# Performance work log

Hardware: AMD Instinct MI355X
Metric: run time of the kernel (lower is better)

## Reference

```python
import jax, jax.numpy as jnp
import numpy as np

PS = 32

def _masks(ps):
    yy, xx = np.meshgrid(np.arange(ps), np.arange(ps), indexing='ij')
    c = (ps - 1) / 2.0
    r = np.sqrt((yy - c) ** 2 + (xx - c) ** 2)
    rm = max(r.max(), 1.0)
    ml = (r <= rm / 3.0).astype(np.float32)
    mm = ((r > rm / 3.0) & (r <= 2.0 * rm / 3.0)).astype(np.float32)
    mh = (r > 2.0 * rm / 3.0).astype(np.float32)
    return jnp.asarray(ml), jnp.asarray(mm), jnp.asarray(mh)

MASK_L, MASK_M, MASK_H = _masks(PS)

def setup_inputs() -> dict:
    key = jax.random.key(0)
    ks = jax.random.split(key, 4)
    B, C, H, W = 16, 3, 256, 256
    d = PS * PS            # 1024
    hidden = int(d * 1.5)  # 1536
    c_f = 64
    return {
        'x': jax.random.normal(ks[0], (B, C, H, W), dtype=jnp.float32),
        'W1': jax.random.normal(ks[1], (d, hidden), dtype=jnp.float32) * 0.02,
        'b1': jnp.zeros((hidden,), jnp.float32),
        'W2': jax.random.normal(ks[2], (hidden, d), dtype=jnp.float32) * 0.02,
        'b2': jnp.zeros((d,), jnp.float32),
        'w_proj': jax.random.normal(ks[3], (c_f,), dtype=jnp.float32) * 0.5,
        'gamma': jnp.ones((c_f,), jnp.float32),
        'beta': jnp.zeros((c_f,), jnp.float32),
        'lf_gate': jnp.float32(0.33),
        'mf_gate': jnp.float32(0.34),
        'hf_gate': jnp.float32(0.33),
    }

def _forward(x, W1, b1, W2, b2, w_proj, gamma, beta, lf_gate, mf_gate, hf_gate):
    B, C, H, W = x.shape
    ps = PS
    gh, gw = H // ps, W // ps
    L = gh * gw
    # grayscale
    xg = 0.299 * x[:, 0] + 0.587 * x[:, 1] + 0.114 * x[:, 2]  # [B,H,W]
    # non-overlapping patchify (H,W multiples of ps -> no padding)
    pr = xg.reshape(B, gh, ps, gw, ps).transpose(0, 1, 3, 2, 4).reshape(B, L, ps, ps)
    # per-patch orthonormal FFT2 and magnitude
    mag = jnp.abs(jnp.fft.fft2(pr, norm='ortho'))  # [B,L,ps,ps]
    gate = (jax.nn.sigmoid(lf_gate) * MASK_L
            + jax.nn.sigmoid(mf_gate) * MASK_M
            + jax.nn.sigmoid(hf_gate) * MASK_H)
    mag = mag * gate
    mag_vec = mag.reshape(B * L, ps * ps)
    attn = jax.nn.sigmoid(jax.nn.relu(mag_vec @ W1 + b1) @ W2 + b2)
    mod = mag_vec * attn
    w = mod.mean(axis=-1).reshape(B, L, 1, 1)  # per-patch scalar weight
    recon = pr * (1.0 + w)
    # fold back (exact inverse of the reshape patchify)
    x_rec = recon.reshape(B, gh, gw, ps, ps).transpose(0, 1, 3, 2, 4).reshape(B, H, W)
    # 1x1 conv (1 -> c_f channels, no bias)
    out = x_rec[:, None, :, :] * w_proj[None, :, None, None]  # [B,c_f,H,W]
    # BatchNorm2d (training mode: batch stats, biased variance)
    mean = out.mean(axis=(0, 2, 3), keepdims=True)
    var = out.var(axis=(0, 2, 3), keepdims=True)
    out = (out - mean) * jax.lax.rsqrt(var + 1e-5)
    out = out * gamma[None, :, None, None] + beta[None, :, None, None]
    return jax.nn.relu(out)

def reference(x, W1, b1, W2, b2, w_proj, gamma, beta, lf_gate, mf_gate, hf_gate):
    return _forward(x, W1, b1, W2, b2, w_proj, gamma, beta, lf_gate, mf_gate, hf_gate)
```

## Files before the change

### kernel.cpp

```cpp
#include <hip/hip_runtime.h>
#include <hip/hip_bf16.h>
#include <math.h>

typedef __attribute__((ext_vector_type(8))) short bf16x8;
typedef __attribute__((ext_vector_type(4))) float f32x4;
typedef __attribute__((ext_vector_type(4))) unsigned short u16x4;

static __device__ __forceinline__ float bf2f(unsigned short u) {
    union { unsigned int i; float f; } v; v.i = ((unsigned int)u) << 16; return v.f;
}
static __device__ __forceinline__ unsigned short f2bf(float f) {
    union { float f; unsigned int i; } v; v.f = f;
    unsigned int x = v.i;
    return (unsigned short)((x + 0x7fffu + ((x >> 16) & 1u)) >> 16);
}
static __device__ __forceinline__ float sigmoidf(float v) {
    return 1.0f / (1.0f + expf(-v));
}
static __device__ __forceinline__ void gload16(const unsigned short* g, unsigned short* l) {
    __builtin_amdgcn_global_load_lds(
        (const __attribute__((address_space(1))) unsigned int*)g,
        (__attribute__((address_space(3))) unsigned int*)l, 16, 0, 0);
}

__global__ __launch_bounds__(256) void kpatch(
    const float* __restrict__ x, const float* __restrict__ lf,
    const float* __restrict__ mf, const float* __restrict__ hf,
    float* __restrict__ pr_out, unsigned short* __restrict__ mag_bf,
    float* __restrict__ ppsum, float* __restrict__ ppsq)
{
    __shared__ float sX[32][36];
    __shared__ float sYr[32][36];
    __shared__ float sYi[32][36];
    __shared__ float tc[32], ts[32];
    __shared__ float red_s[4], red_q[4];

    const int t = threadIdx.x;
    const int p = blockIdx.x;
    const int b = p >> 6, l = p & 63;
    const int gy = l >> 3, gx = l & 7;
    const int lane = t & 63, wave = t >> 6;

    if (t < 32) {
        float ang = (float)t * 0.19634954084936207f;
        tc[t] = cosf(ang);
        ts[t] = sinf(ang);
    }

    const int y  = t >> 3;
    const int xc = (t & 7) * 4;
    const int h  = gy * 32 + y;
    const int wbase = gx * 32 + xc;
    const long long idx0 = ((long long)(b * 3 + 0) * 256 + h) * 256 + wbase;
    const long long idx1 = ((long long)(b * 3 + 1) * 256 + h) * 256 + wbase;
    const long long idx2 = ((long long)(b * 3 + 2) * 256 + h) * 256 + wbase;
    float4 r4 = *(const float4*)(x + idx0);
    float4 g4 = *(const float4*)(x + idx1);
    float4 b4 = *(const float4*)(x + idx2);
    float4 gray;
    gray.x = 0.299f * r4.x + 0.587f * g4.x + 0.114f * b4.x;
    gray.y = 0.299f * r4.y + 0.587f * g4.y + 0.114f * b4.y;
    gray.z = 0.299f * r4.z + 0.587f * g4.z + 0.114f * b4.z;
    gray.w = 0.299f * r4.w + 0.587f * g4.w + 0.114f * b4.w;
    *(float4*)&sX[y][xc] = gray;
    *(float4*)(pr_out + p * 1024 + t * 4) = gray;

    float ls = gray.x + gray.y + gray.z + gray.w;
    float lq = gray.x * gray.x + gray.y * gray.y + gray.z * gray.z + gray.w * gray.w;
    #pragma unroll
    for (int off = 32; off > 0; off >>= 1) {
        ls += __shfl_down(ls, off, 64);
        lq += __shfl_down(lq, off, 64);
    }
    if (lane == 0) { red_s[wave] = ls; red_q[wave] = lq; }
    __syncthreads();
    if (t == 0) {
        ppsum[p] = red_s[0] + red_s[1] + red_s[2] + red_s[3];
        ppsq[p]  = red_q[0] + red_q[1] + red_q[2] + red_q[3];
    }

    {
        const int k  = t >> 3;
        const int c0 = (t & 7) * 4;
        float yr[4] = {0,0,0,0}, yi[4] = {0,0,0,0};
        for (int n = 0; n < 32; n++) {
            int wi = (k * n) & 31;
            float cw = tc[wi], sw = ts[wi];
            float4 xv = *(const float4*)&sX[n][c0];
            yr[0] += cw * xv.x; yi[0] -= sw * xv.x;
            yr[1] += cw * xv.y; yi[1] -= sw * xv.y;
            yr[2] += cw * xv.z; yi[2] -= sw * xv.z;
            yr[3] += cw * xv.w; yi[3] -= sw * xv.w;
        }
        *(float4*)&sYr[k][c0] = *(float4*)yr;
        *(float4*)&sYi[k][c0] = *(float4*)yi;
    }
    __syncthreads();

    {
        const int k  = t >> 3;
        const int m0 = (t & 7) * 4;
        float zr[4] = {0,0,0,0}, zi[4] = {0,0,0,0};
        for (int c = 0; c < 32; c++) {
            float yr = sYr[k][c];
            float yi = sYi[k][c];
            #pragma unroll
            for (int j = 0; j < 4; j++) {
                int wi = ((m0 + j) * c) & 31;
                float cw = tc[wi], sw = ts[wi];
                zr[j] += yr * cw + yi * sw;
                zi[j] += yi * cw - yr * sw;
            }
        }
        const float sl = sigmoidf(lf[0]);
        const float sm = sigmoidf(mf[0]);
        const float sh = sigmoidf(hf[0]);
        const float T1 = 480.5f / 9.0f;
        const float T2 = 4.0f * 480.5f / 9.0f;
        const float fk = (float)k - 15.5f;
        u16x4 outv;
        #pragma unroll
        for (int j = 0; j < 4; j++) {
            float fm = (float)(m0 + j) - 15.5f;
            float r2 = fk * fk + fm * fm;
            float g = (r2 <= T1) ? sl : ((r2 <= T2) ? sm : sh);
            float magv = sqrtf(zr[j] * zr[j] + zi[j] * zi[j]) * 0.03125f * g;
            outv[j] = f2bf(magv);
        }
        *(u16x4*)(mag_bf + p * 1024 + k * 32 + m0) = outv;
    }
}

__global__ __launch_bounds__(256) void kconvall(
    const float* __restrict__ W1, const float* __restrict__ W2,
    unsigned short* __restrict__ w1t, unsigned short* __restrict__ w2t)
{
    __shared__ float tile[32][33];
    int id = blockIdx.x;
    const float* W; unsigned short* WT; int K, N, k0, n0;
    if (id < 1536) {
        W = W1; WT = w1t; K = 1024; N = 1536;
        k0 = (id & 31) * 32; n0 = (id >> 5) * 32;
    } else {
        id -= 1536;
        W = W2; WT = w2t; K = 1536; N = 1024;
        k0 = (id % 48) * 32; n0 = (id / 48) * 32;
    }
    const int tx = threadIdx.x & 31, ty = threadIdx.x >> 5;
    #pragma unroll
    for (int i = 0; i < 4; i++) {
        int r = ty + i * 8;
        tile[r][tx] = W[(long long)(k0 + r) * N + n0 + tx];
    }
    __syncthreads();
    #pragma unroll
    for (int i = 0; i < 4; i++) {
        int r = ty + i * 8;
        WT[(long long)(n0 + r) * K + k0 + tx] = f2bf(tile[tx][r]);
    }
}

__global__ __launch_bounds__(256) void kgemm1(
    const unsigned short* __restrict__ A, const unsigned short* __restrict__ BT,
    const float* __restrict__ bias, unsigned short* __restrict__ C)
{
    const int K = 1024, N = 1536;
    __shared__ unsigned short sA[64 * 64];
    __shared__ unsigned short sB[64 * 64];

    const int t = threadIdx.x;
    const int lane = t & 63, wave = t >> 6;
    const int wm = wave & 1, wn = wave >> 1;
    const int m0 = blockIdx.x * 64, n0 = blockIdx.y * 64;

    const int u0 = t, u1 = t + 256;
    const int r0 = u0 >> 3, c0 = (u0 & 7) ^ (r0 & 7);
    const int r1 = u1 >> 3, c1 = (u1 & 7) ^ (r1 & 7);
    const unsigned short* agp0 = A  + (long long)(m0 + r0) * K + c0 * 8;
    const unsigned short* agp1 = A  + (long long)(m0 + r1) * K + c1 * 8;
    const unsigned short* bgp0 = BT + (long long)(n0 + r0) * K + c0 * 8;
    const unsigned short* bgp1 = BT + (long long)(n0 + r1) * K + c1 * 8;
    unsigned short* al0 = sA + u0 * 8;
    unsigned short* al1 = sA + u1 * 8;
    unsigned short* bl0 = sB + u0 * 8;
    unsigned short* bl1 = sB + u1 * 8;

    const int lr = lane & 15, quad = lane >> 4;
    const int ra0 = wm * 32 + lr, ra1 = ra0 + 16;
    const int rb0 = wn * 32 + lr, rb1 = rb0 + 16;
    const int ea = ra0 & 7, eb = rb0 & 7;

    f32x4 acc00 = {0,0,0,0}, acc01 = {0,0,0,0}, acc10 = {0,0,0,0}, acc11 = {0,0,0,0};

    for (int kk = 0; kk < K; kk += 64) {
        __syncthreads();
        gload16(agp0 + kk, al0);
        gload16(agp1 + kk, al1);
        gload16(bgp0 + kk, bl0);
        gload16(bgp1 + kk, bl1);
        __syncthreads();
        #pragma unroll
        for (int st = 0; st < 2; st++) {
            const int cq = st * 4 + quad;
            bf16x8 a0 = *(const bf16x8*)(sA + ra0 * 64 + ((cq ^ ea) << 3));
            bf16x8 a1 = *(const bf16x8*)(sA + ra1 * 64 + ((cq ^ ea) << 3));
            bf16x8 b0 = *(const bf16x8*)(sB + rb0 * 64 + ((cq ^ eb) << 3));
            bf16x8 b1 = *(const bf16x8*)(sB + rb1 * 64 + ((cq ^ eb) << 3));
            acc00 = __builtin_amdgcn_mfma_f32_16x16x32_bf16(a0, b0, acc00, 0, 0, 0);
            acc01 = __builtin_amdgcn_mfma_f32_16x16x32_bf16(a0, b1, acc01, 0, 0, 0);
            acc10 = __builtin_amdgcn_mfma_f32_16x16x32_bf16(a1, b0, acc10, 0, 0, 0);
            acc11 = __builtin_amdgcn_mfma_f32_16x16x32_bf16(a1, b1, acc11, 0, 0, 0);
        }
    }

    const int col0 = n0 + wn * 32 + lr, col1 = col0 + 16;
    const float bias0 = bias[col0], bias1 = bias[col1];
    const int row0b = m0 + wm * 32 + quad * 4;
    #pragma unroll
    for (int r = 0; r < 4; r++) {
        int row0 = row0b + r, row1 = row0 + 16;
        C[(long long)row0 * N + col0] = f2bf(fmaxf(acc00[r] + bias0, 0.0f));
        C[(long long)row0 * N + col1] = f2bf(fmaxf(acc01[r] + bias1, 0.0f));
        C[(long long)row1 * N + col0] = f2bf(fmaxf(acc10[r] + bias0, 0.0f));
        C[(long long)row1 * N + col1] = f2bf(fmaxf(acc11[r] + bias1, 0.0f));
    }
}

__global__ __launch_bounds__(256) void kgemm2d(
    const unsigned short* __restrict__ A, const unsigned short* __restrict__ BT,
    const float* __restrict__ bias, const unsigned short* __restrict__ mag,
    float* __restrict__ wpart)
{
    const int K = 1536;
    __shared__ unsigned short sA[64 * 64];
    __shared__ unsigned short sB[64 * 64];

    const int t = threadIdx.x;
    const int lane = t & 63, wave = t >> 6;
    const int wm = wave & 1, wn = wave >> 1;
    const int m0 = blockIdx.x * 64, n0 = blockIdx.y * 64;

    const int u0 = t, u1 = t + 256;
    const int r0 = u0 >> 3, c0 = (u0 & 7) ^ (r0 & 7);
    const int r1 = u1 >> 3, c1 = (u1 & 7) ^ (r1 & 7);
    const unsigned short* agp0 = A  + (long long)(m0 + r0) * K + c0 * 8;
    const unsigned short* agp1 = A  + (long long)(m0 + r1) * K + c1 * 8;
    const unsigned short* bgp0 = BT + (long long)(n0 + r0) * K + c0 * 8;
    const unsigned short* bgp1 = BT + (long long)(n0 + r1) * K + c1 * 8;
    unsigned short* al0 = sA + u0 * 8;
    unsigned short* al1 = sA + u1 * 8;
    unsigned short* bl0 = sB + u0 * 8;
    unsigned short* bl1 = sB + u1 * 8;

    const int lr = lane & 15, quad = lane >> 4;
    const int ra0 = wm * 32 + lr, ra1 = ra0 + 16;
    const int rb0 = wn * 32 + lr, rb1 = rb0 + 16;
    const int ea = ra0 & 7, eb = rb0 & 7;

    f32x4 acc00 = {0,0,0,0}, acc01 = {0,0,0,0}, acc10 = {0,0,0,0}, acc11 = {0,0,0,0};

    for (int kk = 0; kk < K; kk += 64) {
        __syncthreads();
        gload16(agp0 + kk, al0);
        gload16(agp1 + kk, al1);
        gload16(bgp0 + kk, bl0);
        gload16(bgp1 + kk, bl1);
        __syncthreads();
        #pragma unroll
        for (int st = 0; st < 2; st++) {
            const int cq = st * 4 + quad;
            bf16x8 a0 = *(const bf16x8*)(sA + ra0 * 64 + ((cq ^ ea) << 3));
            bf16x8 a1 = *(const bf16x8*)(sA + ra1 * 64 + ((cq ^ ea) << 3));
            bf16x8 b0 = *(const bf16x8*)(sB + rb0 * 64 + ((cq ^ eb) << 3));
            bf16x8 b1 = *(const bf16x8*)(sB + rb1 * 64 + ((cq ^ eb) << 3));
            acc00 = __builtin_amdgcn_mfma_f32_16x16x32_bf16(a0, b0, acc00, 0, 0, 0);
            acc01 = __builtin_amdgcn_mfma_f32_16x16x32_bf16(a0, b1, acc01, 0, 0, 0);
            acc10 = __builtin_amdgcn_mfma_f32_16x16x32_bf16(a1, b0, acc10, 0, 0, 0);
            acc11 = __builtin_amdgcn_mfma_f32_16x16x32_bf16(a1, b1, acc11, 0, 0, 0);
        }
    }

    const int col0 = n0 + wn * 32 + lr, col1 = col0 + 16;
    const float bias0 = bias[col0], bias1 = bias[col1];
    const int row0b = m0 + wm * 32 + quad * 4;

    float dsum0[4], dsum1[4];
    #pragma unroll
    for (int r = 0; r < 4; r++) {
        int row0 = row0b + r, row1 = row0 + 16;
        float v00 = sigmoidf(acc00[r] + bias0);
        float v01 = sigmoidf(acc01[r] + bias1);
        float v10 = sigmoidf(acc10[r] + bias0);
        float v11 = sigmoidf(acc11[r] + bias1);
        float m00 = bf2f(mag[(long long)row0 * 1024 + col0]);
        float m01 = bf2f(mag[(long long)row0 * 1024 + col1]);
        float m10 = bf2f(mag[(long long)row1 * 1024 + col0]);
        float m11 = bf2f(mag[(long long)row1 * 1024 + col1]);
        dsum0[r] = m00 * v00 + m01 * v01;
        dsum1[r] = m10 * v10 + m11 * v11;
    }
    #pragma unroll
    for (int r = 0; r < 4; r++) {
        #pragma unroll
        for (int mask = 8; mask > 0; mask >>= 1) {
            dsum0[r] += __shfl_xor(dsum0[r], mask, 64);
            dsum1[r] += __shfl_xor(dsum1[r], mask, 64);
        }
    }
    if (lr == 0) {
        const int cp = blockIdx.y * 2 + wn;
        #pragma unroll
        for (int r = 0; r < 4; r++) {
            wpart[(row0b + r) * 32 + cp]      = dsum0[r];
            wpart[(row0b + 16 + r) * 32 + cp] = dsum1[r];
        }
    }
}

__global__ __launch_bounds__(1024) void kfin(
    const float* __restrict__ wpart, const float* __restrict__ ppsum,
    const float* __restrict__ ppsq, const float* __restrict__ w_proj,
    const float* __restrict__ gamma, const float* __restrict__ beta,
    float* __restrict__ scales, float* __restrict__ der)
{
    __shared__ float rs[16], rq[16];
    const int p = threadIdx.x;
    const int lane = p & 63, wave = p >> 6;

    const float4* wp4 = (const float4*)(wpart + p * 32);
    float w = 0.0f;
    #pragma unroll
    for (int j = 0; j < 8; j++) {
        float4 v = wp4[j];
        w += v.x + v.y + v.z + v.w;
    }
    float scale = 1.0f + w * (1.0f / 1024.0f);
    scales[p] = scale;

    float s = scale * ppsum[p];
    float q = scale * scale * ppsq[p];
    #pragma unroll
    for (int off = 32; off > 0; off >>= 1) {
        s += __shfl_down(s, off, 64);
        q += __shfl_down(q, off, 64);
    }
    if (lane == 0) { rs[wave] = s; rq[wave] = q; }
    __syncthreads();
    if (p < 64) {
        float S = (p < 16) ? rs[p] : 0.0f;
        float Q = (p < 16) ? rq[p] : 0.0f;
        #pragma unroll
        for (int off = 8; off > 0; off >>= 1) {
            S += __shfl_down(S, off, 64);
            Q += __shfl_down(Q, off, 64);
        }
        S = __shfl(S, 0, 64);
        Q = __shfl(Q, 0, 64);
        const float invN = 1.0f / 1048576.0f;
        float mu  = S * invN;
        float var = Q * invN - mu * mu;
        float wp = w_proj[p];
        float A = wp * gamma[p] / sqrtf(wp * wp * var + 1e-5f);
        der[p]      = A;
        der[64 + p] = beta[p] - A * mu;
    }
}

__global__ __launch_bounds__(256) void kout(
    const float* __restrict__ pr, const float* __restrict__ scales,
    const float* __restrict__ der, float* __restrict__ out)
{
    const int total4 = 16777216;
    for (int i4 = blockIdx.x * 256 + threadIdx.x; i4 < total4; i4 += gridDim.x * 256) {
        const int w4 = i4 & 63;
        const int h = (i4 >> 6) & 255;
        const int plane = i4 >> 14;
        const int c = plane & 63;
        const int b = plane >> 6;
        const int p = (b << 6) + ((h >> 5) << 3) + (w4 >> 3);
        const int off4 = ((h & 31) << 3) + (w4 & 7);
        const float As = der[c] * scales[p];
        const float D2 = der[64 + c];
        float4 v = ((const float4*)pr)[p * 256 + off4];
        f32x4 o;
        o[0] = fmaxf(fmaf(As, v.x, D2), 0.0f);
        o[1] = fmaxf(fmaf(As, v.y, D2), 0.0f);
        o[2] = fmaxf(fmaf(As, v.z, D2), 0.0f);
        o[3] = fmaxf(fmaf(As, v.w, D2), 0.0f);
        __builtin_nontemporal_store(o, (f32x4*)out + i4);
    }
}

extern "C" void kernel_launch(void* const* d_in, const int* in_sizes, int n_in,
                              void* d_out, int out_size, void* d_ws, size_t ws_size,
                              hipStream_t stream)
{
    const float* x      = (const float*)d_in[0];
    const float* W1     = (const float*)d_in[1];
    const float* b1     = (const float*)d_in[2];
    const float* W2     = (const float*)d_in[3];
    const float* b2     = (const float*)d_in[4];
    const float* w_proj = (const float*)d_in[5];
    const float* gamma  = (const float*)d_in[6];
    const float* beta   = (const float*)d_in[7];
    const float* lf     = (const float*)d_in[8];
    const float* mf     = (const float*)d_in[9];
    const float* hf     = (const float*)d_in[10];

    char* ws = (char*)d_ws;
    float* pr                 = (float*)(ws);
    unsigned short* mag_bf    = (unsigned short*)(ws + (4u<<20));
    unsigned short* hidden_bf = (unsigned short*)(ws + (6u<<20));
    unsigned short* w1t       = (unsigned short*)(ws + (10u<<20));
    unsigned short* w2t       = (unsigned short*)(ws + (13u<<20));
    float* wpart              = (float*)(ws + (16u<<20));
    float* ppsum              = (float*)(ws + (17u<<20));
    float* ppsq               = (float*)(ws + (17u<<20) + 4096);
    float* scales             = (float*)(ws + (17u<<20) + 8192);
    float* der                = (float*)(ws + (17u<<20) + 12288);

    kconvall<<<3072, 256, 0, stream>>>(W1, W2, w1t, w2t);
    kpatch<<<1024, 256, 0, stream>>>(x, lf, mf, hf, pr, mag_bf, ppsum, ppsq);
    kgemm1<<<dim3(16, 24), 256, 0, stream>>>(mag_bf, w1t, b1, hidden_bf);
    kgemm2d<<<dim3(16, 16), 256, 0, stream>>>(hidden_bf, w2t, b2, mag_bf, wpart);
    kfin<<<1, 1024, 0, stream>>>(wpart, ppsum, ppsq, w_proj, gamma, beta, scales, der);
    kout<<<2048, 256, 0, stream>>>(pr, scales, der, (float*)d_out);
}
```

Baseline: 349.4 us.

## Merge weight conversion into patch kernel and double-buffer GEMM LDS tiles

Folds the W1/W2 transpose-to-bf16 conversion into the patch/FFT kernel as extra blocks, which removes one kernel launch and lets the two independent jobs run concurrently. Both GEMMs now double-buffer their shared-memory A/B tiles, issuing the next K-tile's global-to-LDS loads before computing on the current tile, so each iteration needs one barrier instead of two. This doubles LDS use per block, which may reduce occupancy. The merged kernel reuses the patch kernel's shared buffer as the transpose tile.

```diff
diff --git a/kernel.cpp b/kernel.cpp
--- a/kernel.cpp
+++ b/kernel.cpp
@@ -23,11 +23,13 @@
         (__attribute__((address_space(3))) unsigned int*)l, 16, 0, 0);
 }
 
-__global__ __launch_bounds__(256) void kpatch(
+__global__ __launch_bounds__(256) void kprep(
     const float* __restrict__ x, const float* __restrict__ lf,
     const float* __restrict__ mf, const float* __restrict__ hf,
+    const float* __restrict__ W1, const float* __restrict__ W2,
     float* __restrict__ pr_out, unsigned short* __restrict__ mag_bf,
-    float* __restrict__ ppsum, float* __restrict__ ppsq)
+    float* __restrict__ ppsum, float* __restrict__ ppsq,
+    unsigned short* __restrict__ w1t, unsigned short* __restrict__ w2t)
 {
     __shared__ float sX[32][36];
     __shared__ float sYr[32][36];
@@ -36,7 +38,36 @@
     __shared__ float red_s[4], red_q[4];
 
     const int t = threadIdx.x;
-    const int p = blockIdx.x;
+    const int bid = blockIdx.x;
+
+    if (bid >= 1024) {
+        int id = bid - 1024;
+        float (*tile)[33] = (float (*)[33])(&sX[0][0]);
+        const float* W; unsigned short* WT; int K, N, k0, n0;
+        if (id < 1536) {
+            W = W1; WT = w1t; K = 1024; N = 1536;
+            k0 = (id & 31) * 32; n0 = (id >> 5) * 32;
+        } else {
+            id -= 1536;
+            W = W2; WT = w2t; K = 1536; N = 1024;
+            k0 = (id % 48) * 32; n0 = (id / 48) * 32;
+        }
+        const int tx = t & 31, ty = t >> 5;
+        #pragma unroll
+        for (int i = 0; i < 4; i++) {
+            int r = ty + i * 8;
+            tile[r][tx] = W[(long long)(k0 + r) * N + n0 + tx];
+        }
+        __syncthreads();
+        #pragma unroll
+        for (int i = 0; i < 4; i++) {
+            int r = ty + i * 8;
+            WT[(long long)(n0 + r) * K + k0 + tx] = f2bf(tile[tx][r]);
+        }
+        return;
+    }
+
+    const int p = bid;
     const int b = p >> 6, l = p & 63;
     const int gy = l >> 3, gx = l & 7;
     const int lane = t & 63, wave = t >> 6;
@@ -131,42 +162,13 @@
     }
 }
 
-__global__ __launch_bounds__(256) void kconvall(
-    const float* __restrict__ W1, const float* __restrict__ W2,
-    unsigned short* __restrict__ w1t, unsigned short* __restrict__ w2t)
-{
-    __shared__ float tile[32][33];
-    int id = blockIdx.x;
-    const float* W; unsigned short* WT; int K, N, k0, n0;
-    if (id < 1536) {
-        W = W1; WT = w1t; K = 1024; N = 1536;
-        k0 = (id & 31) * 32; n0 = (id >> 5) * 32;
-    } else {
-        id -= 1536;
-        W = W2; WT = w2t; K = 1536; N = 1024;
-        k0 = (id % 48) * 32; n0 = (id / 48) * 32;
-    }
-    const int tx = threadIdx.x & 31, ty = threadIdx.x >> 5;
-    #pragma unroll
-    for (int i = 0; i < 4; i++) {
-        int r = ty + i * 8;
-        tile[r][tx] = W[(long long)(k0 + r) * N + n0 + tx];
-    }
-    __syncthreads();
-    #pragma unroll
-    for (int i = 0; i < 4; i++) {
-        int r = ty + i * 8;
-        WT[(long long)(n0 + r) * K + k0 + tx] = f2bf(tile[tx][r]);
-    }
-}
-
 __global__ __launch_bounds__(256) void kgemm1(
     const unsigned short* __restrict__ A, const unsigned short* __restrict__ BT,
     const float* __restrict__ bias, unsigned short* __restrict__ C)
 {
     const int K = 1024, N = 1536;
-    __shared__ unsigned short sA[64 * 64];
-    __shared__ unsigned short sB[64 * 64];
+    __shared__ unsigned short sA[2][64 * 64];
+    __shared__ unsigned short sB[2][64 * 64];
 
     const int t = threadIdx.x;
     const int lane = t & 63, wave = t >> 6;
@@ -180,10 +182,6 @@
     const unsigned short* agp1 = A  + (long long)(m0 + r1) * K + c1 * 8;
     const unsigned short* bgp0 = BT + (long long)(n0 + r0) * K + c0 * 8;
     const unsigned short* bgp1 = BT + (long long)(n0 + r1) * K + c1 * 8;
-    unsigned short* al0 = sA + u0 * 8;
-    unsigned short* al1 = sA + u1 * 8;
-    unsigned short* bl0 = sB + u0 * 8;
-    unsigned short* bl1 = sB + u1 * 8;
 
     const int lr = lane & 15, quad = lane >> 4;
     const int ra0 = wm * 32 + lr, ra1 = ra0 + 16;
@@ -192,25 +190,37 @@
 
     f32x4 acc00 = {0,0,0,0}, acc01 = {0,0,0,0}, acc10 = {0,0,0,0}, acc11 = {0,0,0,0};
 
+    gload16(agp0, sA[0] + u0 * 8);
+    gload16(agp1, sA[0] + u1 * 8);
+    gload16(bgp0, sB[0] + u0 * 8);
+    gload16(bgp1, sB[0] + u1 * 8);
+    __syncthreads();
+
+    int buf = 0;
     for (int kk = 0; kk < K; kk += 64) {
-        __syncthreads();
-        gload16(agp0 + kk, al0);
-        gload16(agp1 + kk, al1);
-        gload16(bgp0 + kk, bl0);
-        gload16(bgp1 + kk, bl1);
-        __syncthreads();
+        const int nx = kk + 64;
+        if (nx < K) {
+            gload16(agp0 + nx, sA[buf ^ 1] + u0 * 8);
+            gload16(agp1 + nx, sA[buf ^ 1] + u1 * 8);
+            gload16(bgp0 + nx, sB[buf ^ 1] + u0 * 8);
+            gload16(bgp1 + nx, sB[buf ^ 1] + u1 * 8);
+        }
+        const unsigned short* cA = sA[buf];
+        const unsigned short* cB = sB[buf];
         #pragma unroll
         for (int st = 0; st < 2; st++) {
             const int cq = st * 4 + quad;
-            bf16x8 a0 = *(const bf16x8*)(sA + ra0 * 64 + ((cq ^ ea) << 3));
-            bf16x8 a1 = *(const bf16x8*)(sA + ra1 * 64 + ((cq ^ ea) << 3));
-            bf16x8 b0 = *(const bf16x8*)(sB + rb0 * 64 + ((cq ^ eb) << 3));
-            bf16x8 b1 = *(const bf16x8*)(sB + rb1 * 64 + ((cq ^ eb) << 3));
+            bf16x8 a0 = *(const bf16x8*)(cA + ra0 * 64 + ((cq ^ ea) << 3));
+            bf16x8 a1 = *(const bf16x8*)(cA + ra1 * 64 + ((cq ^ ea) << 3));
+            bf16x8 b0 = *(const bf16x8*)(cB + rb0 * 64 + ((cq ^ eb) << 3));
+            bf16x8 b1 = *(const bf16x8*)(cB + rb1 * 64 + ((cq ^ eb) << 3));
             acc00 = __builtin_amdgcn_mfma_f32_16x16x32_bf16(a0, b0, acc00, 0, 0, 0);
             acc01 = __builtin_amdgcn_mfma_f32_16x16x32_bf16(a0, b1, acc01, 0, 0, 0);
             acc10 = __builtin_amdgcn_mfma_f32_16x16x32_bf16(a1, b0, acc10, 0, 0, 0);
             acc11 = __builtin_amdgcn_mfma_f32_16x16x32_bf16(a1, b1, acc11, 0, 0, 0);
         }
+        __syncthreads();
+        buf ^= 1;
     }
 
     const int col0 = n0 + wn * 32 + lr, col1 = col0 + 16;
@@ -232,8 +242,8 @@
     float* __restrict__ wpart)
 {
     const int K = 1536;
-    __shared__ unsigned short sA[64 * 64];
-    __shared__ unsigned short sB[64 * 64];
+    __shared__ unsigned short sA[2][64 * 64];
+    __shared__ unsigned short sB[2][64 * 64];
 
     const int t = threadIdx.x;
     const int lane = t & 63, wave = t >> 6;
@@ -247,10 +257,6 @@
     const unsigned short* agp1 = A  + (long long)(m0 + r1) * K + c1 * 8;
     const unsigned short* bgp0 = BT + (long long)(n0 + r0) * K + c0 * 8;
     const unsigned short* bgp1 = BT + (long long)(n0 + r1) * K + c1 * 8;
-    unsigned short* al0 = sA + u0 * 8;
-    unsigned short* al1 = sA + u1 * 8;
-    unsigned short* bl0 = sB + u0 * 8;
-    unsigned short* bl1 = sB + u1 * 8;
 
     const int lr = lane & 15, quad = lane >> 4;
     const int ra0 = wm * 32 + lr, ra1 = ra0 + 16;
@@ -259,25 +265,37 @@
 
     f32x4 acc00 = {0,0,0,0}, acc01 = {0,0,0,0}, acc10 = {0,0,0,0}, acc11 = {0,0,0,0};
 
+    gload16(agp0, sA[0] + u0 * 8);
+    gload16(agp1, sA[0] + u1 * 8);
+    gload16(bgp0, sB[0] + u0 * 8);
+    gload16(bgp1, sB[0] + u1 * 8);
+    __syncthreads();
+
+    int buf = 0;
     for (int kk = 0; kk < K; kk += 64) {
-        __syncthreads();
-        gload16(agp0 + kk, al0);
-        gload16(agp1 + kk, al1);
-        gload16(bgp0 + kk, bl0);
-        gload16(bgp1 + kk, bl1);
-        __syncthreads();
+        const int nx = kk + 64;
+        if (nx < K) {
+            gload16(agp0 + nx, sA[buf ^ 1] + u0 * 8);
+            gload16(agp1 + nx, sA[buf ^ 1] + u1 * 8);
+            gload16(bgp0 + nx, sB[buf ^ 1] + u0 * 8);
+            gload16(bgp1 + nx, sB[buf ^ 1] + u1 * 8);
+        }
+        const unsigned short* cA = sA[buf];
+        const unsigned short* cB = sB[buf];
         #pragma unroll
         for (int st = 0; st < 2; st++) {
             const int cq = st * 4 + quad;
-            bf16x8 a0 = *(const bf16x8*)(sA + ra0 * 64 + ((cq ^ ea) << 3));
-            bf16x8 a1 = *(const bf16x8*)(sA + ra1 * 64 + ((cq ^ ea) << 3));
-            bf16x8 b0 = *(const bf16x8*)(sB + rb0 * 64 + ((cq ^ eb) << 3));
-            bf16x8 b1 = *(const bf16x8*)(sB + rb1 * 64 + ((cq ^ eb) << 3));
+            bf16x8 a0 = *(const bf16x8*)(cA + ra0 * 64 + ((cq ^ ea) << 3));
+            bf16x8 a1 = *(const bf16x8*)(cA + ra1 * 64 + ((cq ^ ea) << 3));
+            bf16x8 b0 = *(const bf16x8*)(cB + rb0 * 64 + ((cq ^ eb) << 3));
+            bf16x8 b1 = *(const bf16x8*)(cB + rb1 * 64 + ((cq ^ eb) << 3));
             acc00 = __builtin_amdgcn_mfma_f32_16x16x32_bf16(a0, b0, acc00, 0, 0, 0);
             acc01 = __builtin_amdgcn_mfma_f32_16x16x32_bf16(a0, b1, acc01, 0, 0, 0);
             acc10 = __builtin_amdgcn_mfma_f32_16x16x32_bf16(a1, b0, acc10, 0, 0, 0);
             acc11 = __builtin_amdgcn_mfma_f32_16x16x32_bf16(a1, b1, acc11, 0, 0, 0);
         }
+        __syncthreads();
+        buf ^= 1;
     }
 
     const int col0 = n0 + wn * 32 + lr, col1 = col0 + 16;
@@ -419,8 +437,7 @@
     float* scales             = (float*)(ws + (17u<<20) + 8192);
     float* der                = (float*)(ws + (17u<<20) + 12288);
 
-    kconvall<<<3072, 256, 0, stream>>>(W1, W2, w1t, w2t);
-    kpatch<<<1024, 256, 0, stream>>>(x, lf, mf, hf, pr, mag_bf, ppsum, ppsq);
+    kprep<<<4096, 256, 0, stream>>>(x, lf, mf, hf, W1, W2, pr, mag_bf, ppsum, ppsq, w1t, w2t);
     kgemm1<<<dim3(16, 24), 256, 0, stream>>>(mag_bf, w1t, b1, hidden_bf);
     kgemm2d<<<dim3(16, 16), 256, 0, stream>>>(hidden_bf, w2t, b2, mag_bf, wpart);
     kfin<<<1, 1024, 0, stream>>>(wpart, ppsum, ppsq, w_proj, gamma, beta, scales, der);
```

New measurement: 351.9 us. No clear change (+0.7%).
